# Kernel optimization log

Measured on AMD Instinct MI355X. Metric: run time of the kernel, lower is better.

The kernel has to match this reference:

```python
import jax, jax.numpy as jnp
import numpy as np

G, N, D, E, F = 1024, 65536, 128, 400000, 4
HID, N_EDGE_TYPES, DIST_TRUNC = 64, 3, 10
EDGE_REP_DIM = 4 * D + F  # 516


def _mlp(x, W1, b1, W2, b2):
    return jnp.dot(jax.nn.relu(jnp.dot(x, W1) + b1), W2) + b2


def setup_inputs() -> dict:
    key = jax.random.key(0)
    ks = jax.random.split(key, 16)
    feats = jax.random.uniform(ks[6], (E, F), dtype=jnp.float32)
    feats = feats.at[:, 0].multiply(12.0)  # distances in [0, 12) to exercise truncation
    s = 0.05
    return {
        'input_molecule_representations': jax.random.normal(ks[0], (G, D), jnp.float32),
        'partial_graph_representations': jax.random.normal(ks[1], (G, D), jnp.float32),
        'node_representations': jax.random.normal(ks[2], (N, D), jnp.float32),
        'focus_node_idx_in_batch': jax.random.randint(ks[3], (G,), 0, N, jnp.int32),
        'node_to_graph_map': jnp.sort(jax.random.randint(ks[4], (N,), 0, G, jnp.int32)),
        'candidate_edge_targets': jax.random.randint(ks[5], (E,), 0, N, jnp.int32),
        'candidate_edge_features': feats,
        'num_graphs_in_batch': G,
        'dist_emb_table': jax.random.normal(ks[7], (DIST_TRUNC, 1), jnp.float32) * s,
        'no_more_edges_rep': jax.random.normal(ks[8], (1, D + F), jnp.float32) * s,
        'scorer_W1': jax.random.normal(ks[9], (EDGE_REP_DIM, HID), jnp.float32) * s,
        'scorer_b1': jnp.zeros((HID,), jnp.float32),
        'scorer_W2': jax.random.normal(ks[10], (HID, 1), jnp.float32) * s,
        'scorer_b2': jnp.zeros((1,), jnp.float32),
        'type_W1': jax.random.normal(ks[11], (EDGE_REP_DIM, HID), jnp.float32) * s,
        'type_b1': jnp.zeros((HID,), jnp.float32),
        'type_W2': jax.random.normal(ks[12], (HID, N_EDGE_TYPES), jnp.float32) * s,
        'type_b2': jnp.zeros((N_EDGE_TYPES,), jnp.float32),
    }


def reference(input_molecule_representations, partial_graph_representations,
              node_representations, focus_node_idx_in_batch, node_to_graph_map,
              candidate_edge_targets, candidate_edge_features, num_graphs_in_batch,
              dist_emb_table, no_more_edges_rep,
              scorer_W1, scorer_b1, scorer_W2, scorer_b2,
              type_W1, type_b1, type_W2, type_b2):
    # focus node rep per graph: [G, D]
    focus_node_reps = node_representations[focus_node_idx_in_batch]
    # [G, 3D]
    graph_and_focus = jnp.concatenate(
        (input_molecule_representations, partial_graph_representations, focus_node_reps), axis=-1)
    # irregular gathers per edge candidate
    valid_target_to_graph = node_to_graph_map[candidate_edge_targets]      # [E]
    gfn_per_edge = graph_and_focus[valid_target_to_graph]                  # [E, 3D]
    target_reps = node_representations[candidate_edge_targets]            # [E, D]
    trunc_dist = jnp.minimum(candidate_edge_features[:, 0],
                             jnp.float32(DIST_TRUNC - 1)).astype(jnp.int32)
    dist_emb = dist_emb_table[trunc_dist]                                  # [E, 1]
    edge_rep = jnp.concatenate(
        (gfn_per_edge, target_reps, dist_emb, candidate_edge_features[:, 1:]), axis=-1)  # [E, 4D+F]
    stop_rep = jnp.concatenate(
        [graph_and_focus, jnp.tile(no_more_edges_rep, (num_graphs_in_batch, 1))], axis=-1)  # [G, 4D+F]
    all_feats = jnp.concatenate([edge_rep, stop_rep], axis=0)              # [E+G, 4D+F]
    edge_candidate_logits = jnp.squeeze(_mlp(all_feats, scorer_W1, scorer_b1, scorer_W2, scorer_b2), axis=-1)
    edge_type_logits = _mlp(edge_rep, type_W1, type_b1, type_W2, type_b2)  # [E, 3]
    return (edge_candidate_logits, edge_type_logits)
```

## Files before the change

kernel.cpp:

```cpp
#include <hip/hip_runtime.h>

using u16    = unsigned short;
using f32x4  = __attribute__((ext_vector_type(4))) float;
using bf16x8 = __attribute__((ext_vector_type(8))) __bf16;

#define E_CNT 400000
#define G_CNT 1024

#define WS_HND   0u
#define WS_HGF   16777216u
#define WS_WFRAG 17301504u
#define WS_CT    17432576u
#define WS_NMEH  17436672u

__device__ __forceinline__ u16 f2bf(float f) {
  unsigned u = __builtin_bit_cast(unsigned, f);
  return (u16)((u + 0x7fffu + ((u >> 16) & 1u)) >> 16);
}
__device__ __forceinline__ float b2f(u16 v) {
  unsigned u = ((unsigned)v) << 16;
  return __builtin_bit_cast(float, u);
}
__device__ __forceinline__ uint4 pack8(f32x4 a, f32x4 b) {
  uint4 r;
  r.x = (unsigned)f2bf(a[0]) | ((unsigned)f2bf(a[1]) << 16);
  r.y = (unsigned)f2bf(a[2]) | ((unsigned)f2bf(a[3]) << 16);
  r.z = (unsigned)f2bf(b[0]) | ((unsigned)f2bf(b[1]) << 16);
  r.w = (unsigned)f2bf(b[2]) | ((unsigned)f2bf(b[3]) << 16);
  return r;
}
__device__ __forceinline__ float w1c(const float* sW1, const float* tW1, int k, int j) {
  return (j < 64) ? sW1[(size_t)k * 64 + j] : tW1[(size_t)k * 64 + (j - 64)];
}
__device__ __forceinline__ float dpp_red16(float x) {
  int v;
  v = __builtin_amdgcn_update_dpp(0, __builtin_bit_cast(int, x), 0xB1, 0xF, 0xF, false);
  x += __builtin_bit_cast(float, v);
  v = __builtin_amdgcn_update_dpp(0, __builtin_bit_cast(int, x), 0x4E, 0xF, 0xF, false);
  x += __builtin_bit_cast(float, v);
  v = __builtin_amdgcn_update_dpp(0, __builtin_bit_cast(int, x), 0x141, 0xF, 0xF, false);
  x += __builtin_bit_cast(float, v);
  v = __builtin_amdgcn_update_dpp(0, __builtin_bit_cast(int, x), 0x140, 0xF, 0xF, false);
  x += __builtin_bit_cast(float, v);
  return x;
}

__global__ __launch_bounds__(256) void k_prep(const float* __restrict__ nme,
                                              const float* __restrict__ sW1,
                                              const float* __restrict__ tW1,
                                              const float* __restrict__ sW2,
                                              const float* __restrict__ tW2,
                                              u16* __restrict__ wfrag,
                                              float* __restrict__ ct,
                                              float* __restrict__ nmeh) {
  int b = blockIdx.x;
  if (b < 256) {
    int idx = b * 256 + threadIdx.x;
    int j = idx & 7, l = (idx >> 3) & 63, fn = (idx >> 9) & 7, c = idx >> 12;
    int col = fn * 16 + (l & 15);
    int k = c * 32 + (l >> 4) * 8 + j;
    wfrag[idx] = f2bf(w1c(sW1, tW1, k, col));
  } else {
    int p = threadIdx.x;
    if (p >= 128) return;
    int q = p >> 3, i = p & 7, j = i * 16 + q;
    ct[0 * 128 + p] = w1c(sW1, tW1, 513, j);
    ct[1 * 128 + p] = w1c(sW1, tW1, 514, j);
    ct[2 * 128 + p] = w1c(sW1, tW1, 515, j);
    ct[3 * 128 + p] = (i < 4) ? sW2[j] : 0.f;
    if (i >= 4) {
      int jj = j - 64;
      ct[4 * 128 + p] = tW2[jj * 3 + 0];
      ct[5 * 128 + p] = tW2[jj * 3 + 1];
      ct[6 * 128 + p] = tW2[jj * 3 + 2];
    } else {
      ct[4 * 128 + p] = 0.f; ct[5 * 128 + p] = 0.f; ct[6 * 128 + p] = 0.f;
    }
    ct[7 * 128 + p] = w1c(sW1, tW1, 512, j);
    float s = 0.f;
    for (int k = 0; k < 132; ++k) s += nme[k] * w1c(sW1, tW1, 384 + k, j);
    nmeh[p] = s;
  }
}

__global__ __launch_bounds__(64) void k_hgf(const float* __restrict__ imr,
                                            const float* __restrict__ pgr,
                                            const float* __restrict__ nr,
                                            const int* __restrict__ focus,
                                            const u16* __restrict__ wfrag,
                                            const float* __restrict__ sb1,
                                            const float* __restrict__ tb1,
                                            const float* __restrict__ nmeh,
                                            const float* __restrict__ ct,
                                            const float* __restrict__ sb2,
                                            float* __restrict__ hgf,
                                            float* __restrict__ out0) {
  int l = threadIdx.x, lr = l & 15, lg = l >> 4;
  int row0 = blockIdx.x * 16;
  int fo = focus[row0 + lr];
  f32x4 acc[8];
#pragma unroll
  for (int j = 0; j < 8; ++j) acc[j] = (f32x4){0.f, 0.f, 0.f, 0.f};
#pragma unroll
  for (int c2 = 0; c2 < 12; ++c2) {
    const float* ap;
    if (c2 < 4)      ap = imr + (size_t)(row0 + lr) * 128 + c2 * 32;
    else if (c2 < 8) ap = pgr + (size_t)(row0 + lr) * 128 + (c2 - 4) * 32;
    else             ap = nr + (size_t)fo * 128 + (c2 - 8) * 32;
    ap += lg * 8;
    bf16x8 aF = __builtin_bit_cast(bf16x8, pack8(*(const f32x4*)ap, *(const f32x4*)(ap + 4)));
    bf16x8 bF[8];
#pragma unroll
    for (int fn = 0; fn < 8; ++fn)
      bF[fn] = *(const bf16x8*)((const char*)wfrag + (size_t)(c2 * 8 + fn) * 1024 + l * 16);
#pragma unroll
    for (int fn = 0; fn < 8; ++fn)
      acc[fn] = __builtin_amdgcn_mfma_f32_16x16x32_bf16(aF, bF[fn], acc[fn], 0, 0, 0);
  }
  f32x4 sb1v, tb1v;
#pragma unroll
  for (int fn = 0; fn < 4; ++fn) {
    sb1v[fn] = sb1[fn * 16 + lr];
    tb1v[fn] = tb1[fn * 16 + lr];
  }
  f32x4 nmv = *(const f32x4*)(nmeh + lr * 8);
  f32x4 w2v = *(const f32x4*)(ct + 3 * 128 + lr * 8);
  float sb2v = sb2[0];
#pragma unroll
  for (int rg = 0; rg < 4; ++rg) {
    int g = row0 + lg * 4 + rg;
    f32x4 v0, v1;
#pragma unroll
    for (int fn = 0; fn < 4; ++fn) v0[fn] = acc[fn][rg] + sb1v[fn];
#pragma unroll
    for (int fn = 0; fn < 4; ++fn) v1[fn] = acc[fn + 4][rg] + tb1v[fn];
    *(f32x4*)(hgf + (size_t)g * 128 + lr * 8) = v0;
    *(f32x4*)(hgf + (size_t)g * 128 + lr * 8 + 4) = v1;
    float sp = 0.f;
#pragma unroll
    for (int i = 0; i < 4; ++i) sp += fmaxf(v0[i] + nmv[i], 0.f) * w2v[i];
#pragma unroll
    for (int m = 1; m < 16; m <<= 1) sp += __shfl_xor(sp, m, 64);
    if (lr == 0) out0[E_CNT + g] = sp + sb2v;
  }
}

__global__ __launch_bounds__(64) void k_hnode(const float* __restrict__ nr,
                                              const u16* __restrict__ wfrag,
                                              const int* __restrict__ n2g,
                                              const float* __restrict__ hgf,
                                              u16* __restrict__ hnode) {
  int l = threadIdx.x, lr = l & 15, lg = l >> 4;
  int row0 = blockIdx.x * 16;
  f32x4 acc[8];
#pragma unroll
  for (int j = 0; j < 8; ++j) acc[j] = (f32x4){0.f, 0.f, 0.f, 0.f};
#pragma unroll
  for (int c2 = 0; c2 < 4; ++c2) {
    const float* ap = nr + (size_t)(row0 + lr) * 128 + c2 * 32 + lg * 8;
    bf16x8 aF = __builtin_bit_cast(bf16x8, pack8(*(const f32x4*)ap, *(const f32x4*)(ap + 4)));
    bf16x8 bF[8];
#pragma unroll
    for (int fn = 0; fn < 8; ++fn)
      bF[fn] = *(const bf16x8*)((const char*)wfrag + (size_t)((12 + c2) * 8 + fn) * 1024 + l * 16);
#pragma unroll
    for (int fn = 0; fn < 8; ++fn)
      acc[fn] = __builtin_amdgcn_mfma_f32_16x16x32_bf16(aF, bF[fn], acc[fn], 0, 0, 0);
  }
#pragma unroll
  for (int rg = 0; rg < 4; ++rg) {
    int m = row0 + lg * 4 + rg;
    int g = n2g[m];
    f32x4 v0 = *(const f32x4*)(hgf + (size_t)g * 128 + lr * 8);
    f32x4 v1 = *(const f32x4*)(hgf + (size_t)g * 128 + lr * 8 + 4);
    f32x4 s0, s1;
#pragma unroll
    for (int i = 0; i < 4; ++i) { s0[i] = acc[i][rg] + v0[i]; s1[i] = acc[i + 4][rg] + v1[i]; }
    *(uint4*)(hnode + (size_t)m * 128 + lr * 8) = pack8(s0, s1);
  }
}

__global__ __launch_bounds__(256) void k_edge(
    const u16* __restrict__ hnode, const float* __restrict__ ct,
    const int* __restrict__ tgt, const float4* __restrict__ feats,
    const float* __restrict__ dtab, const float* __restrict__ sb2,
    const float* __restrict__ tb2, float* __restrict__ out0,
    float* __restrict__ out1) {
  int tid = threadIdx.x;
  int q = tid & 15;
  int e0 = blockIdx.x * 64 + (tid >> 4) * 4;

  f32x4 wf1a = *(const f32x4*)(ct + 0 * 128 + q * 8), wf1b = *(const f32x4*)(ct + 0 * 128 + q * 8 + 4);
  f32x4 wf2a = *(const f32x4*)(ct + 1 * 128 + q * 8), wf2b = *(const f32x4*)(ct + 1 * 128 + q * 8 + 4);
  f32x4 wf3a = *(const f32x4*)(ct + 2 * 128 + q * 8), wf3b = *(const f32x4*)(ct + 2 * 128 + q * 8 + 4);
  f32x4 w2v  = *(const f32x4*)(ct + 3 * 128 + q * 8);
  f32x4 tw0v = *(const f32x4*)(ct + 4 * 128 + q * 8 + 4);
  f32x4 tw1v = *(const f32x4*)(ct + 5 * 128 + q * 8 + 4);
  f32x4 tw2v = *(const f32x4*)(ct + 6 * 128 + q * 8 + 4);
  f32x4 w5a  = *(const f32x4*)(ct + 7 * 128 + q * 8), w5b = *(const f32x4*)(ct + 7 * 128 + q * 8 + 4);
  float sb2v = sb2[0], tb0 = tb2[0], tb1 = tb2[1], tb2s = tb2[2];

  int t[4];
#pragma unroll
  for (int j = 0; j < 4; ++j) t[j] = tgt[e0 + j];
  float4 f[4];
#pragma unroll
  for (int j = 0; j < 4; ++j) f[j] = feats[e0 + j];
  union { uint4 v; u16 s[8]; } hn[4];
#pragma unroll
  for (int j = 0; j < 4; ++j)
    hn[j].v = *(const uint4*)(hnode + (size_t)t[j] * 128 + q * 8);
  float fd[4];
#pragma unroll
  for (int j = 0; j < 4; ++j) fd[j] = dtab[(int)fminf(f[j].x, 9.f)];

  float sc[4], t0[4], t1[4], t2[4];
#pragma unroll
  for (int j = 0; j < 4; ++j) {
    float s = 0.f, a0 = 0.f, a1 = 0.f, a2 = 0.f;
#pragma unroll
    for (int i = 0; i < 4; ++i) {
      float h = b2f(hn[j].s[i]) + fd[j] * w5a[i] + f[j].y * wf1a[i] + f[j].z * wf2a[i] + f[j].w * wf3a[i];
      s += fmaxf(h, 0.f) * w2v[i];
    }
#pragma unroll
    for (int i = 0; i < 4; ++i) {
      float h = b2f(hn[j].s[4 + i]) + fd[j] * w5b[i] + f[j].y * wf1b[i] + f[j].z * wf2b[i] + f[j].w * wf3b[i];
      float r = fmaxf(h, 0.f);
      a0 += r * tw0v[i]; a1 += r * tw1v[i]; a2 += r * tw2v[i];
    }
    sc[j] = s; t0[j] = a0; t1[j] = a1; t2[j] = a2;
  }
#pragma unroll
  for (int j = 0; j < 4; ++j) {
    sc[j] = dpp_red16(sc[j]); t0[j] = dpp_red16(t0[j]);
    t1[j] = dpp_red16(t1[j]); t2[j] = dpp_red16(t2[j]);
  }
  if (q == 0) {
    *(float4*)(out0 + e0) = make_float4(sc[0] + sb2v, sc[1] + sb2v, sc[2] + sb2v, sc[3] + sb2v);
    float* o = out1 + (size_t)e0 * 3;
    *(float4*)(o + 0) = make_float4(t0[0] + tb0, t1[0] + tb1, t2[0] + tb2s, t0[1] + tb0);
    *(float4*)(o + 4) = make_float4(t1[1] + tb1, t2[1] + tb2s, t0[2] + tb0, t1[2] + tb1);
    *(float4*)(o + 8) = make_float4(t2[2] + tb2s, t0[3] + tb0, t1[3] + tb1, t2[3] + tb2s);
  }
}

extern "C" void kernel_launch(void* const* d_in, const int* in_sizes, int n_in,
                              void* d_out, int out_size, void* d_ws, size_t ws_size,
                              hipStream_t stream) {
  const float* imr   = (const float*)d_in[0];
  const float* pgr   = (const float*)d_in[1];
  const float* nr    = (const float*)d_in[2];
  const int*   focus = (const int*)d_in[3];
  const int*   n2g   = (const int*)d_in[4];
  const int*   tgt   = (const int*)d_in[5];
  const float* feats = (const float*)d_in[6];
  const float* dtab  = (const float*)d_in[8];
  const float* nme   = (const float*)d_in[9];
  const float* sW1   = (const float*)d_in[10];
  const float* sb1   = (const float*)d_in[11];
  const float* sW2   = (const float*)d_in[12];
  const float* sb2   = (const float*)d_in[13];
  const float* tW1   = (const float*)d_in[14];
  const float* tb1   = (const float*)d_in[15];
  const float* tW2   = (const float*)d_in[16];
  const float* tb2   = (const float*)d_in[17];

  char* ws = (char*)d_ws;
  u16*   HND   = (u16*)(ws + WS_HND);
  float* HGF   = (float*)(ws + WS_HGF);
  u16*   WFRAG = (u16*)(ws + WS_WFRAG);
  float* CT    = (float*)(ws + WS_CT);
  float* NMEH  = (float*)(ws + WS_NMEH);

  float* out0 = (float*)d_out;
  float* out1 = out0 + (E_CNT + G_CNT);

  k_prep<<<257, 256, 0, stream>>>(nme, sW1, tW1, sW2, tW2, WFRAG, CT, NMEH);
  k_hgf<<<64, 64, 0, stream>>>(imr, pgr, nr, focus, WFRAG, sb1, tb1, NMEH, CT, sb2, HGF, out0);
  k_hnode<<<4096, 64, 0, stream>>>(nr, WFRAG, n2g, HGF, HND);
  k_edge<<<6250, 256, 0, stream>>>(HND, CT, tgt, (const float4*)feats,
                                   dtab, sb2, tb2, out0, out1);
}
```

Before: 61.73 us.

## Make edge kernel persistent grid-stride with software-prefetched index loads

The edge scoring kernel now launches a fixed grid of 1024 blocks. Each 16-lane group walks edge groups with a grid stride and prefetches the next group's target indices and features while it gathers and computes the current one. This is meant to hide the dependent index-then-gather latency and to cut block launch overhead and the repeated per-block weight loads. In exchange, fewer waves are in flight to hide the random hnode gathers, and register use goes up.

```diff
diff --git a/kernel.cpp b/kernel.cpp
--- a/kernel.cpp
+++ b/kernel.cpp
@@ -6,6 +6,9 @@
 
 #define E_CNT 400000
 #define G_CNT 1024
+#define NGRP  100000
+#define EGRID 1024
+#define ESTR  (EGRID * 16)
 
 #define WS_HND   0u
 #define WS_HGF   16777216u
@@ -186,9 +189,9 @@
     const float* __restrict__ dtab, const float* __restrict__ sb2,
     const float* __restrict__ tb2, float* __restrict__ out0,
     float* __restrict__ out1) {
-  int tid = threadIdx.x;
-  int q = tid & 15;
-  int e0 = blockIdx.x * 64 + (tid >> 4) * 4;
+  const int tid = threadIdx.x;
+  const int q = tid & 15;
+  const int sid = blockIdx.x * 16 + (tid >> 4);
 
   f32x4 wf1a = *(const f32x4*)(ct + 0 * 128 + q * 8), wf1b = *(const f32x4*)(ct + 0 * 128 + q * 8 + 4);
   f32x4 wf2a = *(const f32x4*)(ct + 1 * 128 + q * 8), wf2b = *(const f32x4*)(ct + 1 * 128 + q * 8 + 4);
@@ -200,48 +203,73 @@
   f32x4 w5a  = *(const f32x4*)(ct + 7 * 128 + q * 8), w5b = *(const f32x4*)(ct + 7 * 128 + q * 8 + 4);
   float sb2v = sb2[0], tb0 = tb2[0], tb1 = tb2[1], tb2s = tb2[2];
 
-  int t[4];
-#pragma unroll
-  for (int j = 0; j < 4; ++j) t[j] = tgt[e0 + j];
-  float4 f[4];
-#pragma unroll
-  for (int j = 0; j < 4; ++j) f[j] = feats[e0 + j];
-  union { uint4 v; u16 s[8]; } hn[4];
-#pragma unroll
-  for (int j = 0; j < 4; ++j)
-    hn[j].v = *(const uint4*)(hnode + (size_t)t[j] * 128 + q * 8);
-  float fd[4];
-#pragma unroll
-  for (int j = 0; j < 4; ++j) fd[j] = dtab[(int)fminf(f[j].x, 9.f)];
-
-  float sc[4], t0[4], t1[4], t2[4];
-#pragma unroll
-  for (int j = 0; j < 4; ++j) {
-    float s = 0.f, a0 = 0.f, a1 = 0.f, a2 = 0.f;
-#pragma unroll
-    for (int i = 0; i < 4; ++i) {
-      float h = b2f(hn[j].s[i]) + fd[j] * w5a[i] + f[j].y * wf1a[i] + f[j].z * wf2a[i] + f[j].w * wf3a[i];
-      s += fmaxf(h, 0.f) * w2v[i];
+  auto ldidx = [&](int g, int* t, float4* f) {
+#pragma unroll
+    for (int j = 0; j < 4; ++j) t[j] = tgt[g * 4 + j];
+#pragma unroll
+    for (int j = 0; j < 4; ++j) f[j] = feats[g * 4 + j];
+  };
+  auto ldhn = [&](const int* t, uint4* h) {
+#pragma unroll
+    for (int j = 0; j < 4; ++j)
+      h[j] = *(const uint4*)(hnode + (size_t)t[j] * 128 + q * 8);
+  };
+  auto comp = [&](int g, const float4* f, const uint4* hv) {
+    float sc[4], t0[4], t1[4], t2[4];
+#pragma unroll
+    for (int j = 0; j < 4; ++j) {
+      union { uint4 v; u16 s[8]; } hn;
+      hn.v = hv[j];
+      float fd = dtab[(int)fminf(f[j].x, 9.f)];
+      float s = 0.f, a0 = 0.f, a1 = 0.f, a2 = 0.f;
+#pragma unroll
+      for (int i = 0; i < 4; ++i) {
+        float h = b2f(hn.s[i]) + fd * w5a[i] + f[j].y * wf1a[i] + f[j].z * wf2a[i] + f[j].w * wf3a[i];
+        s += fmaxf(h, 0.f) * w2v[i];
+      }
+#pragma unroll
+      for (int i = 0; i < 4; ++i) {
+        float h = b2f(hn.s[4 + i]) + fd * w5b[i] + f[j].y * wf1b[i] + f[j].z * wf2b[i] + f[j].w * wf3b[i];
+        float r = fmaxf(h, 0.f);
+        a0 += r * tw0v[i]; a1 += r * tw1v[i]; a2 += r * tw2v[i];
+      }
+      sc[j] = s; t0[j] = a0; t1[j] = a1; t2[j] = a2;
     }
 #pragma unroll
-    for (int i = 0; i < 4; ++i) {
-      float h = b2f(hn[j].s[4 + i]) + fd[j] * w5b[i] + f[j].y * wf1b[i] + f[j].z * wf2b[i] + f[j].w * wf3b[i];
-      float r = fmaxf(h, 0.f);
-      a0 += r * tw0v[i]; a1 += r * tw1v[i]; a2 += r * tw2v[i];
+    for (int j = 0; j < 4; ++j) {
+      sc[j] = dpp_red16(sc[j]); t0[j] = dpp_red16(t0[j]);
+      t1[j] = dpp_red16(t1[j]); t2[j] = dpp_red16(t2[j]);
     }
-    sc[j] = s; t0[j] = a0; t1[j] = a1; t2[j] = a2;
-  }
-#pragma unroll
-  for (int j = 0; j < 4; ++j) {
-    sc[j] = dpp_red16(sc[j]); t0[j] = dpp_red16(t0[j]);
-    t1[j] = dpp_red16(t1[j]); t2[j] = dpp_red16(t2[j]);
-  }
-  if (q == 0) {
-    *(float4*)(out0 + e0) = make_float4(sc[0] + sb2v, sc[1] + sb2v, sc[2] + sb2v, sc[3] + sb2v);
-    float* o = out1 + (size_t)e0 * 3;
-    *(float4*)(o + 0) = make_float4(t0[0] + tb0, t1[0] + tb1, t2[0] + tb2s, t0[1] + tb0);
-    *(float4*)(o + 4) = make_float4(t1[1] + tb1, t2[1] + tb2s, t0[2] + tb0, t1[2] + tb1);
-    *(float4*)(o + 8) = make_float4(t2[2] + tb2s, t0[3] + tb0, t1[3] + tb1, t2[3] + tb2s);
+    if (q == 0) {
+      int e0 = g * 4;
+      *(float4*)(out0 + e0) = make_float4(sc[0] + sb2v, sc[1] + sb2v, sc[2] + sb2v, sc[3] + sb2v);
+      float* o = out1 + (size_t)e0 * 3;
+      *(float4*)(o + 0) = make_float4(t0[0] + tb0, t1[0] + tb1, t2[0] + tb2s, t0[1] + tb0);
+      *(float4*)(o + 4) = make_float4(t1[1] + tb1, t2[1] + tb2s, t0[2] + tb0, t1[2] + tb1);
+      *(float4*)(o + 8) = make_float4(t2[2] + tb2s, t0[3] + tb0, t1[3] + tb1, t2[3] + tb2s);
+    }
+  };
+
+  int g0 = sid;
+  int tC[4]; float4 fC[4];
+  ldidx(g0, tC, fC);
+  for (;;) {
+    int g1 = g0 + ESTR;
+    bool has1 = (g1 < NGRP);
+    int tN[4]; float4 fN[4];
+    if (has1) ldidx(g1, tN, fN);
+    uint4 hC[4];
+    ldhn(tC, hC);
+    comp(g0, fC, hC);
+    if (!has1) break;
+    int g2 = g1 + ESTR;
+    bool has2 = (g2 < NGRP);
+    if (has2) ldidx(g2, tC, fC);
+    uint4 hN[4];
+    ldhn(tN, hN);
+    comp(g1, fN, hN);
+    if (!has2) break;
+    g0 = g2;
   }
 }
 
@@ -279,6 +307,6 @@
   k_prep<<<257, 256, 0, stream>>>(nme, sW1, tW1, sW2, tW2, WFRAG, CT, NMEH);
   k_hgf<<<64, 64, 0, stream>>>(imr, pgr, nr, focus, WFRAG, sb1, tb1, NMEH, CT, sb2, HGF, out0);
   k_hnode<<<4096, 64, 0, stream>>>(nr, WFRAG, n2g, HGF, HND);
-  k_edge<<<6250, 256, 0, stream>>>(HND, CT, tgt, (const float4*)feats,
-                                   dtab, sb2, tb2, out0, out1);
-}
+  k_edge<<<EGRID, 256, 0, stream>>>(HND, CT, tgt, (const float4*)feats,
+                                    dtab, sb2, tb2, out0, out1);
+}
```

Result: no change. 62.31 us (+0.9%).

## Bucket edges by target node and fuse node projection with edge scoring

Applied to the files above, without the earlier changes.

Removes the bf16 per-node hidden buffer. Edges are now sorted by target node with a histogram, a single-block scan and an atomic scatter, so one fused kernel computes each node tile's first-layer projection in MFMA registers and then scores all edges whose target falls in that tile. This cuts the write and scattered re-read of the 16 MB hnode intermediate, and keeps the node hidden values in fp32 rather than bf16. In exchange it adds three extra launches with atomics, serial per-wave edge loops with load imbalance across nodes, and scattered single-float output writes.

```diff
diff --git a/kernel.cpp b/kernel.cpp
--- a/kernel.cpp
+++ b/kernel.cpp
@@ -6,20 +6,20 @@
 
 #define E_CNT 400000
 #define G_CNT 1024
-
-#define WS_HND   0u
-#define WS_HGF   16777216u
-#define WS_WFRAG 17301504u
-#define WS_CT    17432576u
-#define WS_NMEH  17436672u
+#define NNODE 65536
+
+#define WS_HGF   0u
+#define WS_WFRAG 524288u
+#define WS_CT    655360u
+#define WS_NMEH  659456u
+#define WS_BINS  660480u
+#define WS_OFFS  922624u
+#define WS_CURS  1184772u
+#define WS_EID   1446916u
 
 __device__ __forceinline__ u16 f2bf(float f) {
   unsigned u = __builtin_bit_cast(unsigned, f);
   return (u16)((u + 0x7fffu + ((u >> 16) & 1u)) >> 16);
-}
-__device__ __forceinline__ float b2f(u16 v) {
-  unsigned u = ((unsigned)v) << 16;
-  return __builtin_bit_cast(float, u);
 }
 __device__ __forceinline__ uint4 pack8(f32x4 a, f32x4 b) {
   uint4 r;
@@ -44,6 +44,11 @@
   x += __builtin_bit_cast(float, v);
   return x;
 }
+__device__ __forceinline__ float sel4(f32x4 a, int rg) {
+  float x01 = (rg & 1) ? a[1] : a[0];
+  float x23 = (rg & 1) ? a[3] : a[2];
+  return (rg & 2) ? x23 : x01;
+}
 
 __global__ __launch_bounds__(256) void k_prep(const float* __restrict__ nme,
                                               const float* __restrict__ sW1,
@@ -52,7 +57,8 @@
                                               const float* __restrict__ tW2,
                                               u16* __restrict__ wfrag,
                                               float* __restrict__ ct,
-                                              float* __restrict__ nmeh) {
+                                              float* __restrict__ nmeh,
+                                              int* __restrict__ bins) {
   int b = blockIdx.x;
   if (b < 256) {
     int idx = b * 256 + threadIdx.x;
@@ -60,7 +66,7 @@
     int col = fn * 16 + (l & 15);
     int k = c * 32 + (l >> 4) * 8 + j;
     wfrag[idx] = f2bf(w1c(sW1, tW1, k, col));
-  } else {
+  } else if (b == 256) {
     int p = threadIdx.x;
     if (p >= 128) return;
     int q = p >> 3, i = p & 7, j = i * 16 + q;
@@ -80,7 +86,63 @@
     float s = 0.f;
     for (int k = 0; k < 132; ++k) s += nme[k] * w1c(sW1, tW1, 384 + k, j);
     nmeh[p] = s;
-  }
+  } else {
+    int idx4 = (b - 257) * 256 + threadIdx.x;
+    *(int4*)(bins + idx4 * 4) = make_int4(0, 0, 0, 0);
+  }
+}
+
+__global__ __launch_bounds__(256) void k_hist(const int* __restrict__ tgt,
+                                              int* __restrict__ bins) {
+  int e = blockIdx.x * 256 + threadIdx.x;
+  if (e < E_CNT) atomicAdd(&bins[tgt[e]], 1);
+}
+
+__global__ __launch_bounds__(1024) void k_scan(const int* __restrict__ bins,
+                                               int* __restrict__ offs,
+                                               int* __restrict__ curs) {
+  __shared__ int wsum[16];
+  int t = threadIdx.x;
+  int b0 = t * 64;
+  int loc[64];
+#pragma unroll
+  for (int k = 0; k < 64; ++k) loc[k] = bins[b0 + k];
+  int s = 0;
+#pragma unroll
+  for (int k = 0; k < 64; ++k) s += loc[k];
+  int lane = t & 63, w = t >> 6;
+  int v = s;
+#pragma unroll
+  for (int d = 1; d < 64; d <<= 1) {
+    int u = __shfl_up(v, d, 64);
+    if (lane >= d) v += u;
+  }
+  if (lane == 63) wsum[w] = v;
+  __syncthreads();
+  if (t == 0) {
+    int a = 0;
+#pragma unroll
+    for (int k = 0; k < 16; ++k) { int x = wsum[k]; wsum[k] = a; a += x; }
+  }
+  __syncthreads();
+  int run = wsum[w] + (v - s);
+#pragma unroll
+  for (int k = 0; k < 64; ++k) {
+    offs[b0 + k] = run;
+    curs[b0 + k] = run;
+    run += loc[k];
+  }
+  if (t == 1023) offs[NNODE] = run;
+}
+
+__global__ __launch_bounds__(256) void k_scatter(const int* __restrict__ tgt,
+                                                 int* __restrict__ curs,
+                                                 int* __restrict__ eid) {
+  int e = blockIdx.x * 256 + threadIdx.x;
+  if (e >= E_CNT) return;
+  int t = tgt[e];
+  int pos = atomicAdd(&curs[t], 1);
+  eid[pos] = e | ((t & 3) << 20);
 }
 
 __global__ __launch_bounds__(64) void k_hgf(const float* __restrict__ imr,
@@ -145,13 +207,18 @@
   }
 }
 
-__global__ __launch_bounds__(64) void k_hnode(const float* __restrict__ nr,
-                                              const u16* __restrict__ wfrag,
-                                              const int* __restrict__ n2g,
-                                              const float* __restrict__ hgf,
-                                              u16* __restrict__ hnode) {
-  int l = threadIdx.x, lr = l & 15, lg = l >> 4;
-  int row0 = blockIdx.x * 16;
+__global__ __launch_bounds__(128) void k_final(
+    const float* __restrict__ nr, const u16* __restrict__ wfrag,
+    const int* __restrict__ n2g, const float* __restrict__ hgf,
+    const int* __restrict__ offs, const int* __restrict__ eid,
+    const float4* __restrict__ feats, const float* __restrict__ dtab,
+    const float* __restrict__ ct, const float* __restrict__ sb2,
+    const float* __restrict__ tb2, float* __restrict__ out0,
+    float* __restrict__ out1) {
+  int tid = threadIdx.x;
+  int w = tid >> 6, l = tid & 63, lr = l & 15, lg = l >> 4;
+  int row0 = blockIdx.x * 32 + w * 16;
+
   f32x4 acc[8];
 #pragma unroll
   for (int j = 0; j < 8; ++j) acc[j] = (f32x4){0.f, 0.f, 0.f, 0.f};
@@ -173,23 +240,11 @@
     int g = n2g[m];
     f32x4 v0 = *(const f32x4*)(hgf + (size_t)g * 128 + lr * 8);
     f32x4 v1 = *(const f32x4*)(hgf + (size_t)g * 128 + lr * 8 + 4);
-    f32x4 s0, s1;
-#pragma unroll
-    for (int i = 0; i < 4; ++i) { s0[i] = acc[i][rg] + v0[i]; s1[i] = acc[i + 4][rg] + v1[i]; }
-    *(uint4*)(hnode + (size_t)m * 128 + lr * 8) = pack8(s0, s1);
-  }
-}
-
-__global__ __launch_bounds__(256) void k_edge(
-    const u16* __restrict__ hnode, const float* __restrict__ ct,
-    const int* __restrict__ tgt, const float4* __restrict__ feats,
-    const float* __restrict__ dtab, const float* __restrict__ sb2,
-    const float* __restrict__ tb2, float* __restrict__ out0,
-    float* __restrict__ out1) {
-  int tid = threadIdx.x;
-  int q = tid & 15;
-  int e0 = blockIdx.x * 64 + (tid >> 4) * 4;
-
+#pragma unroll
+    for (int i = 0; i < 4; ++i) { acc[i][rg] += v0[i]; acc[i + 4][rg] += v1[i]; }
+  }
+
+  int q = lr;
   f32x4 wf1a = *(const f32x4*)(ct + 0 * 128 + q * 8), wf1b = *(const f32x4*)(ct + 0 * 128 + q * 8 + 4);
   f32x4 wf2a = *(const f32x4*)(ct + 1 * 128 + q * 8), wf2b = *(const f32x4*)(ct + 1 * 128 + q * 8 + 4);
   f32x4 wf3a = *(const f32x4*)(ct + 2 * 128 + q * 8), wf3b = *(const f32x4*)(ct + 2 * 128 + q * 8 + 4);
@@ -200,48 +255,39 @@
   f32x4 w5a  = *(const f32x4*)(ct + 7 * 128 + q * 8), w5b = *(const f32x4*)(ct + 7 * 128 + q * 8 + 4);
   float sb2v = sb2[0], tb0 = tb2[0], tb1 = tb2[1], tb2s = tb2[2];
 
-  int t[4];
-#pragma unroll
-  for (int j = 0; j < 4; ++j) t[j] = tgt[e0 + j];
-  float4 f[4];
-#pragma unroll
-  for (int j = 0; j < 4; ++j) f[j] = feats[e0 + j];
-  union { uint4 v; u16 s[8]; } hn[4];
-#pragma unroll
-  for (int j = 0; j < 4; ++j)
-    hn[j].v = *(const uint4*)(hnode + (size_t)t[j] * 128 + q * 8);
-  float fd[4];
-#pragma unroll
-  for (int j = 0; j < 4; ++j) fd[j] = dtab[(int)fminf(f[j].x, 9.f)];
-
-  float sc[4], t0[4], t1[4], t2[4];
-#pragma unroll
-  for (int j = 0; j < 4; ++j) {
-    float s = 0.f, a0 = 0.f, a1 = 0.f, a2 = 0.f;
-#pragma unroll
-    for (int i = 0; i < 4; ++i) {
-      float h = b2f(hn[j].s[i]) + fd[j] * w5a[i] + f[j].y * wf1a[i] + f[j].z * wf2a[i] + f[j].w * wf3a[i];
-      s += fmaxf(h, 0.f) * w2v[i];
+  int base = row0 + lg * 4;
+  int i = offs[base];
+  int end = offs[base + 4];
+  int vc = 0; float4 fc = make_float4(0.f, 0.f, 0.f, 0.f);
+  if (i < end) { vc = eid[i]; fc = feats[vc & 0xFFFFF]; }
+  while (__any(i < end)) {
+    int in_ = i + 1;
+    int vn = 0; float4 fn_ = fc;
+    if (in_ < end) { vn = eid[in_]; fn_ = feats[vn & 0xFFFFF]; }
+    if (i < end) {
+      int e = vc & 0xFFFFF;
+      int rg = (vc >> 20) & 3;
+      float fd = dtab[(int)fminf(fc.x, 9.f)];
+      float s = 0.f, a0 = 0.f, a1 = 0.f, a2 = 0.f;
+#pragma unroll
+      for (int ii = 0; ii < 4; ++ii) {
+        float h = sel4(acc[ii], rg) + fd * w5a[ii] + fc.y * wf1a[ii] + fc.z * wf2a[ii] + fc.w * wf3a[ii];
+        s += fmaxf(h, 0.f) * w2v[ii];
+      }
+#pragma unroll
+      for (int ii = 0; ii < 4; ++ii) {
+        float h = sel4(acc[ii + 4], rg) + fd * w5b[ii] + fc.y * wf1b[ii] + fc.z * wf2b[ii] + fc.w * wf3b[ii];
+        float r = fmaxf(h, 0.f);
+        a0 += r * tw0v[ii]; a1 += r * tw1v[ii]; a2 += r * tw2v[ii];
+      }
+      s = dpp_red16(s); a0 = dpp_red16(a0); a1 = dpp_red16(a1); a2 = dpp_red16(a2);
+      if (lr == 0) {
+        out0[e] = s + sb2v;
+        float* o = out1 + (size_t)e * 3;
+        o[0] = a0 + tb0; o[1] = a1 + tb1; o[2] = a2 + tb2s;
+      }
     }
-#pragma unroll
-    for (int i = 0; i < 4; ++i) {
-      float h = b2f(hn[j].s[4 + i]) + fd[j] * w5b[i] + f[j].y * wf1b[i] + f[j].z * wf2b[i] + f[j].w * wf3b[i];
-      float r = fmaxf(h, 0.f);
-      a0 += r * tw0v[i]; a1 += r * tw1v[i]; a2 += r * tw2v[i];
-    }
-    sc[j] = s; t0[j] = a0; t1[j] = a1; t2[j] = a2;
-  }
-#pragma unroll
-  for (int j = 0; j < 4; ++j) {
-    sc[j] = dpp_red16(sc[j]); t0[j] = dpp_red16(t0[j]);
-    t1[j] = dpp_red16(t1[j]); t2[j] = dpp_red16(t2[j]);
-  }
-  if (q == 0) {
-    *(float4*)(out0 + e0) = make_float4(sc[0] + sb2v, sc[1] + sb2v, sc[2] + sb2v, sc[3] + sb2v);
-    float* o = out1 + (size_t)e0 * 3;
-    *(float4*)(o + 0) = make_float4(t0[0] + tb0, t1[0] + tb1, t2[0] + tb2s, t0[1] + tb0);
-    *(float4*)(o + 4) = make_float4(t1[1] + tb1, t2[1] + tb2s, t0[2] + tb0, t1[2] + tb1);
-    *(float4*)(o + 8) = make_float4(t2[2] + tb2s, t0[3] + tb0, t1[3] + tb1, t2[3] + tb2s);
+    i = in_; vc = vn; fc = fn_;
   }
 }
 
@@ -267,18 +313,23 @@
   const float* tb2   = (const float*)d_in[17];
 
   char* ws = (char*)d_ws;
-  u16*   HND   = (u16*)(ws + WS_HND);
   float* HGF   = (float*)(ws + WS_HGF);
   u16*   WFRAG = (u16*)(ws + WS_WFRAG);
   float* CT    = (float*)(ws + WS_CT);
   float* NMEH  = (float*)(ws + WS_NMEH);
+  int*   BINS  = (int*)(ws + WS_BINS);
+  int*   OFFS  = (int*)(ws + WS_OFFS);
+  int*   CURS  = (int*)(ws + WS_CURS);
+  int*   EID   = (int*)(ws + WS_EID);
 
   float* out0 = (float*)d_out;
   float* out1 = out0 + (E_CNT + G_CNT);
 
-  k_prep<<<257, 256, 0, stream>>>(nme, sW1, tW1, sW2, tW2, WFRAG, CT, NMEH);
+  k_prep<<<321, 256, 0, stream>>>(nme, sW1, tW1, sW2, tW2, WFRAG, CT, NMEH, BINS);
+  k_hist<<<1563, 256, 0, stream>>>(tgt, BINS);
+  k_scan<<<1, 1024, 0, stream>>>(BINS, OFFS, CURS);
+  k_scatter<<<1563, 256, 0, stream>>>(tgt, CURS, EID);
   k_hgf<<<64, 64, 0, stream>>>(imr, pgr, nr, focus, WFRAG, sb1, tb1, NMEH, CT, sb2, HGF, out0);
-  k_hnode<<<4096, 64, 0, stream>>>(nr, WFRAG, n2g, HGF, HND);
-  k_edge<<<6250, 256, 0, stream>>>(HND, CT, tgt, (const float4*)feats,
-                                   dtab, sb2, tb2, out0, out1);
-}
+  k_final<<<2048, 128, 0, stream>>>(nr, WFRAG, n2g, HGF, OFFS, EID,
+                                    (const float4*)feats, dtab, CT, sb2, tb2, out0, out1);
+}
```

Result: slower. 166.9 us (+170.4%).
